# Optimization experiments

Measured on AMD Instinct MI355X. Metric: run time of the kernel, lower is better.

The kernel has to match this reference:

```python
import jax, jax.numpy as jnp
import numpy as np

T, B, I, H = 2048, 64, 256, 256


def setup_inputs() -> dict:
    key = jax.random.key(0)
    k_x, k_w, k_hh = jax.random.split(key, 3)
    x = jax.random.normal(k_x, (T, B, I), dtype=jnp.float32)
    # input-to-hidden weight for the 3 gates [r, z, n], torch GRU layout [3H, I]
    W_ih = jax.random.normal(k_w, (3 * H, I), dtype=jnp.float32) * (1.0 / np.sqrt(H))
    # biases are zero-filled in IndGRU.__init__ but remain parameters
    b_ih = jnp.zeros((3 * H,), dtype=jnp.float32)
    b_hh = jnp.zeros((3 * H,), dtype=jnp.float32)
    # per-unit (diagonal) recurrent weights, uniform(-1, 1), rows = [r, z, n]
    w_hh = jax.random.uniform(k_hh, (3, H), dtype=jnp.float32, minval=-1.0, maxval=1.0)
    return {"x": x, "W_ih": W_ih, "b_ih": b_ih, "b_hh": b_hh, "w_hh": w_hh}


def reference(x, W_ih, b_ih, b_hh, w_hh):
    # x: [T, B, I] time-major (torch GRU default). Diagonal-recurrence GRU:
    # the hidden-to-hidden matmul collapses to an elementwise multiply per gate.
    Bsz = x.shape[1]
    Hsz = w_hh.shape[1]
    # Precompute all input-side gate pre-activations in one big GEMM: [T, B, 3H]
    gx = jnp.einsum('tbi,gi->tbg', x, W_ih) + b_ih
    gxr, gxz, gxn = jnp.split(gx, 3, axis=-1)
    w_hr, w_hz, w_hn = w_hh[0], w_hh[1], w_hh[2]
    b_hr, b_hz, b_hn = jnp.split(b_hh, 3)

    def step(h, g):
        xr, xz, xn = g
        r = jax.nn.sigmoid(xr + w_hr * h + b_hr)
        z = jax.nn.sigmoid(xz + w_hz * h + b_hz)
        n = jnp.tanh(xn + r * (w_hn * h + b_hn))
        h_new = (1.0 - z) * n + z * h
        return h_new, h_new

    h0 = jnp.zeros((Bsz, Hsz), dtype=x.dtype)
    h_n, out = jax.lax.scan(step, h0, (gxr, gxz, gxn))
    # torch GRU returns (output [T,B,H], h_n [num_layers=1, B, H])
    return out, h_n[None]
```

## Files before the change

### kernel.cpp

```cpp
#include <hip/hip_runtime.h>
#include <stdint.h>

#define T_LEN 2048
#define BATCH 64
#define I_DIM 256
#define H_DIM 256
#define N3    768
#define M_ROWS (T_LEN*BATCH)
#define L2E 1.4426950408889634f

typedef _Float16 f16;
typedef __attribute__((ext_vector_type(4))) float  f32x4;
typedef __attribute__((ext_vector_type(4))) unsigned int   u32x4;
typedef __attribute__((ext_vector_type(8))) _Float16 f16x8;
typedef __attribute__((ext_vector_type(4))) _Float16 f16x4;

__global__ void convert_w(const float* __restrict__ W,
                          f16* __restrict__ Whf) {
    int idx = blockIdx.x * 256 + threadIdx.x;
    int row = idx >> 8;
    float scale = (row < 2*H_DIM) ? -L2E : -2.0f*L2E;
    Whf[idx] = (f16)(W[idx] * scale);
}

#define BM 128
#define BN 128
#define BK 64

__device__ __forceinline__ int lds_swz(int row, int kbyte) {
    return row * 128 + (kbyte ^ ((row & 7) << 4));
}

__global__ __launch_bounds__(256, 4) void gemm_gx(
        const float* __restrict__ X,
        const f16* __restrict__ Whf,
        f16* __restrict__ gx) {
    __shared__ f16 sA[BM*BK], sB[BN*BK];

    int wg   = blockIdx.x;
    int orig = (wg & 7) * 768 + (wg >> 3);
    int mblk = orig / 6, nblk = orig - mblk * 6;
    int m0 = mblk * BM, n0 = nblk * BN;

    int tid  = threadIdx.x;
    int lane = tid & 63, wid = tid >> 6;
    int wm = wid >> 1, wn = wid & 1;

    int acol = tid & 15, arow = tid >> 4;
    int bcol = tid & 7,  brow = tid >> 3;

    f32x4 acc[4][4] = {};

    for (int kb = 0; kb < 4; ++kb) {
        f32x4 ra[8];
        u32x4 rb[4];
        #pragma unroll
        for (int p = 0; p < 8; ++p) {
            int row = p*16 + arow;
            ra[p] = *(const f32x4*)(X + (size_t)(m0+row)*I_DIM + kb*BK + acol*4);
        }
        #pragma unroll
        for (int p = 0; p < 4; ++p) {
            int row = p*32 + brow;
            rb[p] = *(const u32x4*)(Whf + (size_t)(n0+row)*I_DIM + kb*BK + bcol*8);
        }
        __syncthreads();
        #pragma unroll
        for (int p = 0; p < 8; ++p) {
            int row = p*16 + arow;
            f16x4 hv;
            #pragma unroll
            for (int e = 0; e < 4; ++e) hv[e] = (f16)ra[p][e];
            *(f16x4*)((char*)sA + lds_swz(row, acol*8)) = hv;
        }
        #pragma unroll
        for (int p = 0; p < 4; ++p) {
            int row = p*32 + brow;
            *(u32x4*)((char*)sB + lds_swz(row, bcol*16)) = rb[p];
        }
        __syncthreads();
        #pragma unroll
        for (int kk = 0; kk < 2; ++kk) {
            f16x8 a[4], b[4];
            #pragma unroll
            for (int mi = 0; mi < 4; ++mi) {
                int row = wm*64 + mi*16 + (lane & 15);
                a[mi] = *(const f16x8*)((const char*)sA + lds_swz(row, kk*64 + (lane >> 4)*16));
            }
            #pragma unroll
            for (int ni = 0; ni < 4; ++ni) {
                int row = wn*64 + ni*16 + (lane & 15);
                b[ni] = *(const f16x8*)((const char*)sB + lds_swz(row, kk*64 + (lane >> 4)*16));
            }
            #pragma unroll
            for (int mi = 0; mi < 4; ++mi)
              #pragma unroll
              for (int ni = 0; ni < 4; ++ni)
                acc[mi][ni] = __builtin_amdgcn_mfma_f32_16x16x32_f16(a[mi], b[ni], acc[mi][ni], 0,0,0);
        }
    }
    #pragma unroll
    for (int mi = 0; mi < 4; ++mi) {
        int rbase = m0 + wm*64 + mi*16 + (lane >> 4)*4;
        #pragma unroll
        for (int ni = 0; ni < 4; ++ni) {
            int col = n0 + wn*64 + ni*16 + (lane & 15);
            #pragma unroll
            for (int j = 0; j < 4; ++j)
                gx[(size_t)(rbase + j)*N3 + col] = (f16)acc[mi][ni][j];
        }
    }
}

__global__ __launch_bounds__(64) void indgru_scan(
        const f16* __restrict__ gx, const float* __restrict__ bih,
        const float* __restrict__ bhh, const float* __restrict__ whh,
        float* __restrict__ out) {
    int lane = threadIdx.x;
    int b = blockIdx.x >> 2;
    int h = (blockIdx.x & 3) * 64 + lane;

    float whr = -L2E  * whh[h];
    float whz = -L2E  * whh[H_DIM + h];
    float whn = -2.0f*L2E * whh[2*H_DIM + h];
    float cr  = -L2E  * (bih[h] + bhh[h]);
    float cz  = -L2E  * (bih[H_DIM+h] + bhh[H_DIM+h]);
    float cn  = -2.0f*L2E * bih[2*H_DIM+h];
    float bhn = -2.0f*L2E * bhh[2*H_DIM+h];

    const size_t sg = (size_t)BATCH * N3;
    const size_t so = (size_t)BATCH * H_DIM;
    const f16* pr = gx + (size_t)b*N3 + h;
    float* po = out + (size_t)b*H_DIM + h;

    f16 Ar[16], Az[16], An[16], Br[16], Bz[16], Bn[16];
    float hv = 0.f;

#define LOAD16(R, Z, N, tblk) do {                                  \
        const f16* _p = pr + (size_t)(tblk)*16*sg;                  \
        _Pragma("unroll")                                           \
        for (int _i = 0; _i < 16; ++_i) {                           \
            R[_i] = _p[0]; Z[_i] = _p[H_DIM]; N[_i] = _p[2*H_DIM];  \
            _p += sg;                                               \
        }                                                           \
    } while (0)

#define PROC16(R, Z, N) do {                                        \
        _Pragma("unroll")                                           \
        for (int _j = 0; _j < 16; ++_j) {                           \
            float ur = (float)R[_j] + cr;                           \
            float uz = (float)Z[_j] + cz;                           \
            float un = (float)N[_j] + cn;                           \
            float er = __builtin_amdgcn_exp2f(fmaf(whr, hv, ur));   \
            float r  = __builtin_amdgcn_rcpf(1.f + er);             \
            float ez = __builtin_amdgcn_exp2f(fmaf(whz, hv, uz));   \
            float z  = __builtin_amdgcn_rcpf(1.f + ez);             \
            float mn = fmaf(whn, hv, bhn);                          \
            float en = __builtin_amdgcn_exp2f(fmaf(r, mn, un));     \
            float q  = __builtin_amdgcn_rcpf(1.f + en);             \
            float hp1 = hv + 1.f;                                   \
            hv = fmaf(z, fmaf(-2.f, q, hp1), fmaf(2.f, q, -1.f));   \
            *po = hv; po += so;                                     \
        }                                                           \
    } while (0)

    LOAD16(Ar, Az, An, 0);
    for (int i = 0; i < 63; ++i) {
        LOAD16(Br, Bz, Bn, 2*i+1);
        PROC16(Ar, Az, An);
        LOAD16(Ar, Az, An, 2*i+2);
        PROC16(Br, Bz, Bn);
    }
    LOAD16(Br, Bz, Bn, 127);
    PROC16(Ar, Az, An);
    PROC16(Br, Bz, Bn);

    out[(size_t)T_LEN * so + (size_t)b*H_DIM + h] = hv;
#undef LOAD16
#undef PROC16
}

extern "C" void kernel_launch(void* const* d_in, const int* in_sizes, int n_in,
                              void* d_out, int out_size, void* d_ws, size_t ws_size,
                              hipStream_t stream) {
    const float* x   = (const float*)d_in[0];
    const float* Wih = (const float*)d_in[1];
    const float* bih = (const float*)d_in[2];
    const float* bhh = (const float*)d_in[3];
    const float* whh = (const float*)d_in[4];
    float* out = (float*)d_out;

    char* ws = (char*)d_ws;
    f16* gxbuf = (f16*)ws;
    f16* Whf = (f16*)(ws + (size_t)M_ROWS*N3*sizeof(f16));

    convert_w<<<(N3*I_DIM)/256, 256, 0, stream>>>(Wih, Whf);
    gemm_gx<<<(M_ROWS/BM)*(N3/BN), 256, 0, stream>>>(x, Whf, gxbuf);
    indgru_scan<<<BATCH*(H_DIM/64), 64, 0, stream>>>(gxbuf, bih, bhh, whh, out);
}
```

Baseline: 583.6 us.

## Interleave four timesteps in gate buffer and restructure GEMM with async B loads

The GEMM now writes the gate pre-activations in a layout that packs four consecutive timesteps per (batch, gate) element. The scan kernel can then fetch them as 8-byte vector loads instead of scalar 2-byte loads, which cuts the number of strided memory requests on the serial recurrence. The GEMM also changes to 256x128 tiles with 512 threads and BK=32. It double-buffers the weight tile through direct global-to-LDS loads, uses a new rotation swizzle pre-applied in the weight conversion, and stages output through LDS for coalesced stores. The trade-offs are more LDS use and extra synchronisation in the GEMM epilogue.

```diff
diff --git a/kernel.cpp b/kernel.cpp
--- a/kernel.cpp
+++ b/kernel.cpp
@@ -11,109 +11,114 @@
 
 typedef _Float16 f16;
 typedef __attribute__((ext_vector_type(4))) float  f32x4;
-typedef __attribute__((ext_vector_type(4))) unsigned int   u32x4;
+typedef __attribute__((ext_vector_type(4))) _Float16 f16x4;
 typedef __attribute__((ext_vector_type(8))) _Float16 f16x8;
-typedef __attribute__((ext_vector_type(4))) _Float16 f16x4;
-
-__global__ void convert_w(const float* __restrict__ W,
-                          f16* __restrict__ Whf) {
+
+__global__ void convert_w(const float* __restrict__ W, f16* __restrict__ Whf) {
     int idx = blockIdx.x * 256 + threadIdx.x;
-    int row = idx >> 8;
-    float scale = (row < 2*H_DIM) ? -L2E : -2.0f*L2E;
-    Whf[idx] = (f16)(W[idx] * scale);
-}
-
-#define BM 128
+    int r = idx >> 8, c = idx & 255;
+    float scale = (r < 2*H_DIM) ? -L2E : -2.0f*L2E;
+    int chunk = c >> 5, lu = (c >> 3) & 3, e = c & 7;
+    int pu = (lu + (r >> 1)) & 3;
+    Whf[r*256 + chunk*32 + pu*8 + e] = (f16)(W[idx] * scale);
+}
+
+#define BM 256
 #define BN 128
-#define BK 64
-
-__device__ __forceinline__ int lds_swz(int row, int kbyte) {
-    return row * 128 + (kbyte ^ ((row & 7) << 4));
-}
-
-__global__ __launch_bounds__(256, 4) void gemm_gx(
+#define BK 32
+
+__global__ __launch_bounds__(512, 4) void gemm_gx(
         const float* __restrict__ X,
         const f16* __restrict__ Whf,
-        f16* __restrict__ gx) {
-    __shared__ f16 sA[BM*BK], sB[BN*BK];
+        f16* __restrict__ gxP) {
+    __shared__ union {
+        struct { f16 A[BM*BK]; f16 B[2][BN*BK]; } s;
+        f16 C[64*128*4];
+    } u;
 
     int wg   = blockIdx.x;
-    int orig = (wg & 7) * 768 + (wg >> 3);
+    int orig = (wg & 7) * 384 + (wg >> 3);
     int mblk = orig / 6, nblk = orig - mblk * 6;
     int m0 = mblk * BM, n0 = nblk * BN;
 
-    int tid  = threadIdx.x;
-    int lane = tid & 63, wid = tid >> 6;
+    int tid = threadIdx.x, lane = tid & 63, wid = tid >> 6;
     int wm = wid >> 1, wn = wid & 1;
-
-    int acol = tid & 15, arow = tid >> 4;
-    int bcol = tid & 7,  brow = tid >> 3;
+    int arow = tid >> 3, acol = tid & 7;
 
     f32x4 acc[4][4] = {};
 
-    for (int kb = 0; kb < 4; ++kb) {
-        f32x4 ra[8];
-        u32x4 rb[4];
-        #pragma unroll
-        for (int p = 0; p < 8; ++p) {
-            int row = p*16 + arow;
-            ra[p] = *(const f32x4*)(X + (size_t)(m0+row)*I_DIM + kb*BK + acol*4);
-        }
+    auto issueB = [&](int kb, int buf) {
+        int lrow = wid * 16 + (lane >> 2);
+        const f16* g = Whf + (size_t)(n0 + lrow) * 256 + kb * 32 + (lane & 3) * 8;
+        f16* l = &u.s.B[buf][wid * 16 * BK];
+        __builtin_amdgcn_global_load_lds(
+            (const __attribute__((address_space(1))) void*)g,
+            (__attribute__((address_space(3))) void*)l, 16, 0, 0);
+    };
+
+    issueB(0, 0);
+    int cur = 0;
+    for (int kb = 0; kb < 8; ++kb) {
+        f32x4 ra[4];
+        #pragma unroll
+        for (int p = 0; p < 4; ++p)
+            ra[p] = *(const f32x4*)(X + (size_t)(m0 + p*64 + arow) * I_DIM + kb*BK + acol*4);
+        __syncthreads();
         #pragma unroll
         for (int p = 0; p < 4; ++p) {
-            int row = p*32 + brow;
-            rb[p] = *(const u32x4*)(Whf + (size_t)(n0+row)*I_DIM + kb*BK + bcol*8);
-        }
-        __syncthreads();
-        #pragma unroll
-        for (int p = 0; p < 8; ++p) {
-            int row = p*16 + arow;
+            int row = p*64 + arow;
             f16x4 hv;
             #pragma unroll
             for (int e = 0; e < 4; ++e) hv[e] = (f16)ra[p][e];
-            *(f16x4*)((char*)sA + lds_swz(row, acol*8)) = hv;
-        }
-        #pragma unroll
-        for (int p = 0; p < 4; ++p) {
-            int row = p*32 + brow;
-            *(u32x4*)((char*)sB + lds_swz(row, bcol*16)) = rb[p];
+            int pu = ((acol >> 1) + (row >> 1)) & 3;
+            *(f16x4*)((char*)u.s.A + row*64 + pu*16 + (acol & 1)*8) = hv;
         }
         __syncthreads();
-        #pragma unroll
-        for (int kk = 0; kk < 2; ++kk) {
-            f16x8 a[4], b[4];
-            #pragma unroll
-            for (int mi = 0; mi < 4; ++mi) {
-                int row = wm*64 + mi*16 + (lane & 15);
-                a[mi] = *(const f16x8*)((const char*)sA + lds_swz(row, kk*64 + (lane >> 4)*16));
-            }
-            #pragma unroll
-            for (int ni = 0; ni < 4; ++ni) {
-                int row = wn*64 + ni*16 + (lane & 15);
-                b[ni] = *(const f16x8*)((const char*)sB + lds_swz(row, kk*64 + (lane >> 4)*16));
-            }
-            #pragma unroll
-            for (int mi = 0; mi < 4; ++mi)
-              #pragma unroll
-              for (int ni = 0; ni < 4; ++ni)
-                acc[mi][ni] = __builtin_amdgcn_mfma_f32_16x16x32_f16(a[mi], b[ni], acc[mi][ni], 0,0,0);
-        }
-    }
+        if (kb < 7) issueB(kb + 1, cur ^ 1);
+        f16x8 af[4], bf[4];
+        #pragma unroll
+        for (int mi = 0; mi < 4; ++mi) {
+            int lrow = wm*64 + mi*16 + (lane & 15);
+            int pu = ((lane >> 4) + (lrow >> 1)) & 3;
+            af[mi] = *(const f16x8*)((const char*)u.s.A + lrow*64 + pu*16);
+        }
+        #pragma unroll
+        for (int ni = 0; ni < 4; ++ni) {
+            int lrow = wn*64 + ni*16 + (lane & 15);
+            int pu = ((lane >> 4) + (lrow >> 1)) & 3;
+            bf[ni] = *(const f16x8*)((const char*)u.s.B[cur] + lrow*64 + pu*16);
+        }
+        #pragma unroll
+        for (int mi = 0; mi < 4; ++mi)
+          #pragma unroll
+          for (int ni = 0; ni < 4; ++ni)
+            acc[mi][ni] = __builtin_amdgcn_mfma_f32_16x16x32_f16(af[mi], bf[ni], acc[mi][ni], 0,0,0);
+        cur ^= 1;
+    }
+
+    __syncthreads();
     #pragma unroll
     for (int mi = 0; mi < 4; ++mi) {
-        int rbase = m0 + wm*64 + mi*16 + (lane >> 4)*4;
+        int bb0 = mi*16 + (lane >> 4)*4;
         #pragma unroll
         for (int ni = 0; ni < 4; ++ni) {
-            int col = n0 + wn*64 + ni*16 + (lane & 15);
+            int c = wn*64 + ni*16 + (lane & 15);
             #pragma unroll
             for (int j = 0; j < 4; ++j)
-                gx[(size_t)(rbase + j)*N3 + col] = (f16)acc[mi][ni][j];
-        }
+                u.C[(bb0 + j)*512 + c*4 + wm] = (f16)acc[mi][ni][j];
+        }
+    }
+    __syncthreads();
+    #pragma unroll
+    for (int i = 0; i < 8; ++i) {
+        int idx = i*512 + tid, bb = idx >> 6, w = idx & 63;
+        f16x8 v = *(const f16x8*)&u.C[bb*512 + w*8];
+        *(f16x8*)(gxP + ((size_t)(mblk*64 + bb)*N3 + n0)*4 + w*8) = v;
     }
 }
 
 __global__ __launch_bounds__(64) void indgru_scan(
-        const f16* __restrict__ gx, const float* __restrict__ bih,
+        const f16* __restrict__ gxP, const float* __restrict__ bih,
         const float* __restrict__ bhh, const float* __restrict__ whh,
         float* __restrict__ out) {
     int lane = threadIdx.x;
@@ -128,29 +133,33 @@
     float cn  = -2.0f*L2E * bih[2*H_DIM+h];
     float bhn = -2.0f*L2E * bhh[2*H_DIM+h];
 
-    const size_t sg = (size_t)BATCH * N3;
-    const size_t so = (size_t)BATCH * H_DIM;
-    const f16* pr = gx + (size_t)b*N3 + h;
-    float* po = out + (size_t)b*H_DIM + h;
-
-    f16 Ar[16], Az[16], An[16], Br[16], Bz[16], Bn[16];
+    const size_t stb = (size_t)BATCH * N3 * 4;
+    const size_t so  = (size_t)BATCH * H_DIM;
+    const f16* pr = gxP + ((size_t)b * N3 + h) * 4;
+    float* po = out + (size_t)b * H_DIM + h;
+
+    f16x4 Ar[4], Az[4], An[4], Br[4], Bz[4], Bn[4];
     float hv = 0.f;
 
-#define LOAD16(R, Z, N, tblk) do {                                  \
-        const f16* _p = pr + (size_t)(tblk)*16*sg;                  \
+#define LOADG(R, Z, N, grp) do {                                    \
+        const f16* _p = pr + (size_t)(grp) * 4 * stb;               \
         _Pragma("unroll")                                           \
-        for (int _i = 0; _i < 16; ++_i) {                           \
-            R[_i] = _p[0]; Z[_i] = _p[H_DIM]; N[_i] = _p[2*H_DIM];  \
-            _p += sg;                                               \
+        for (int _q = 0; _q < 4; ++_q) {                            \
+            R[_q] = *(const f16x4*)(_p);                            \
+            Z[_q] = *(const f16x4*)(_p + H_DIM*4);                  \
+            N[_q] = *(const f16x4*)(_p + 2*H_DIM*4);                \
+            _p += stb;                                              \
         }                                                           \
     } while (0)
 
 #define PROC16(R, Z, N) do {                                        \
         _Pragma("unroll")                                           \
-        for (int _j = 0; _j < 16; ++_j) {                           \
-            float ur = (float)R[_j] + cr;                           \
-            float uz = (float)Z[_j] + cz;                           \
-            float un = (float)N[_j] + cn;                           \
+        for (int _q = 0; _q < 4; ++_q)                              \
+        _Pragma("unroll")                                           \
+        for (int _j = 0; _j < 4; ++_j) {                            \
+            float ur = (float)R[_q][_j] + cr;                       \
+            float uz = (float)Z[_q][_j] + cz;                       \
+            float un = (float)N[_q][_j] + cn;                       \
             float er = __builtin_amdgcn_exp2f(fmaf(whr, hv, ur));   \
             float r  = __builtin_amdgcn_rcpf(1.f + er);             \
             float ez = __builtin_amdgcn_exp2f(fmaf(whz, hv, uz));   \
@@ -164,19 +173,19 @@
         }                                                           \
     } while (0)
 
-    LOAD16(Ar, Az, An, 0);
+    LOADG(Ar, Az, An, 0);
     for (int i = 0; i < 63; ++i) {
-        LOAD16(Br, Bz, Bn, 2*i+1);
+        LOADG(Br, Bz, Bn, 2*i + 1);
         PROC16(Ar, Az, An);
-        LOAD16(Ar, Az, An, 2*i+2);
+        LOADG(Ar, Az, An, 2*i + 2);
         PROC16(Br, Bz, Bn);
     }
-    LOAD16(Br, Bz, Bn, 127);
+    LOADG(Br, Bz, Bn, 127);
     PROC16(Ar, Az, An);
     PROC16(Br, Bz, Bn);
 
-    out[(size_t)T_LEN * so + (size_t)b*H_DIM + h] = hv;
-#undef LOAD16
+    out[(size_t)T_LEN * so + (size_t)b * H_DIM + h] = hv;
+#undef LOADG
 #undef PROC16
 }
 
@@ -191,10 +200,10 @@
     float* out = (float*)d_out;
 
     char* ws = (char*)d_ws;
-    f16* gxbuf = (f16*)ws;
-    f16* Whf = (f16*)(ws + (size_t)M_ROWS*N3*sizeof(f16));
+    f16* gxP = (f16*)ws;
+    f16* Whf = (f16*)(ws + (size_t)M_ROWS * N3 * sizeof(f16));
 
     convert_w<<<(N3*I_DIM)/256, 256, 0, stream>>>(Wih, Whf);
-    gemm_gx<<<(M_ROWS/BM)*(N3/BN), 256, 0, stream>>>(x, Whf, gxbuf);
-    indgru_scan<<<BATCH*(H_DIM/64), 64, 0, stream>>>(gxbuf, bih, bhh, whh, out);
-}
+    gemm_gx<<<(M_ROWS/BM)*(N3/BN), 512, 0, stream>>>(x, Whf, gxP);
+    indgru_scan<<<BATCH*(H_DIM/64), 64, 0, stream>>>(gxP, bih, bhh, whh, out);
+}
```

Measured after the change: 518.0 us. -11.2%, faster.
